# Kernel optimization log

Measured on AMD Instinct MI355X. Metric: run time of the kernel, lower is better.

The kernel has to match this reference:

```python
import jax, jax.numpy as jnp
import numpy as np

N = 50000
E = 800000
IN_DIM = 256
H1, D1 = 4, 128   # layer1: 4 heads x 128 = 512 concat
H2, D2 = 1, 256   # layer2: 1 head x 256
NEG_SLOPE = 0.2


def setup_inputs() -> dict:
    key = jax.random.key(0)
    ks = jax.random.split(key, 12)
    feat = jax.random.normal(ks[0], (N, IN_DIM), dtype=jnp.float32)
    src1 = jax.random.randint(ks[1], (E,), 0, N)
    dst1 = jax.random.randint(ks[2], (E,), 0, N)
    src2 = jax.random.randint(ks[3], (E,), 0, N)
    dst2 = jax.random.randint(ks[4], (E,), 0, N)
    s1 = 1.0 / np.sqrt(IN_DIM)
    s2 = 1.0 / np.sqrt(H1 * D1)
    W1 = jax.random.normal(ks[5], (IN_DIM, H1 * D1), dtype=jnp.float32) * s1
    al1 = jax.random.normal(ks[6], (H1, D1), dtype=jnp.float32) * s1
    ar1 = jax.random.normal(ks[7], (H1, D1), dtype=jnp.float32) * s1
    W2 = jax.random.normal(ks[8], (H1 * D1, H2 * D2), dtype=jnp.float32) * s2
    al2 = jax.random.normal(ks[9], (H2, D2), dtype=jnp.float32) * s2
    ar2 = jax.random.normal(ks[10], (H2, D2), dtype=jnp.float32) * s2
    return {"feat": feat, "src1": src1, "dst1": dst1, "src2": src2,
            "dst2": dst2, "W1": W1, "al1": al1, "ar1": ar1,
            "W2": W2, "al2": al2, "ar2": ar2}


def gat_layer(x, W, al, ar, src, dst, heads):
    n = x.shape[0]
    h = (x @ W).reshape(n, heads, -1)               # [N,H,D]
    el = jnp.einsum('nhd,hd->nh', h, al)            # attention left term
    er = jnp.einsum('nhd,hd->nh', h, ar)            # attention right term
    e = jax.nn.leaky_relu(el[src] + er[dst], NEG_SLOPE)   # [E,H]
    # segment softmax over edges grouped by destination node
    m = jax.ops.segment_max(e, dst, num_segments=n)
    m = jax.lax.stop_gradient(jnp.where(jnp.isfinite(m), m, 0.0))
    ee = jnp.exp(e - m[dst])
    s = jax.ops.segment_sum(ee, dst, num_segments=n)
    alpha = ee / (s[dst] + 1e-9)                    # [E,H]
    msg = h[src] * alpha[:, :, None]                # [E,H,D]
    return jax.ops.segment_sum(msg, dst, num_segments=n)  # [N,H,D]


def reference(feat, src1, dst1, src2, dst2, W1, al1, ar1, W2, al2, ar2):
    h1 = gat_layer(feat, W1, al1, ar1, src1, dst1, H1)      # [N,4,128]
    h1 = jax.nn.elu(h1.reshape(N, H1 * D1))                 # concat heads + act
    z = gat_layer(h1, W2, al2, ar2, src2, dst2, H2)         # [N,1,256]
    return z.reshape(N, D2)                                 # no act on last layer
```

## Files before the change

kernel.cpp:

```cpp
#include <hip/hip_runtime.h>
#include <stdint.h>

#define NN 50000
#define EE 800000
#define IND 256
#define HD1 512
#define D2C 256

#define NB1 782
#define NB  (2 * NB1)
#define CH  16384
#define WGN ((2 * EE + CH - 1) / CH)
#define TOT (NB * WGN)
#define SB2 ((TOT + 255) / 256)

#define Q_SCALE 21.166666f
#define Q_INV   0.047244094f

typedef float f32x4 __attribute__((ext_vector_type(4)));
typedef __bf16 bf16x8 __attribute__((ext_vector_type(8)));

__device__ inline float bf2f(unsigned int u) {
    union { unsigned int i; float f; } c; c.i = u << 16; return c.f;
}
__device__ inline unsigned int f2bf(float f) {
    union { float f; unsigned int i; } c; c.f = f;
    unsigned int x = c.i;
    return (x + 0x7FFFu + ((x >> 16) & 1u)) >> 16;
}
__device__ inline float loadf(const void* p, int idx, int isbf) {
    return isbf ? bf2f(((const unsigned short*)p)[idx]) : ((const float*)p)[idx];
}
__device__ inline unsigned int f2q8(float v) {
    float t = fminf(fmaxf(v * Q_SCALE, -127.f), 127.f);
    int q = (int)rintf(t);
    return (unsigned int)q & 0xFFu;
}
__device__ inline void unpack8_q8(uint2 q, float* o) {
    o[0] = (float)(int)(signed char)(q.x & 0xFFu);
    o[1] = (float)(int)(signed char)((q.x >> 8) & 0xFFu);
    o[2] = (float)(int)(signed char)((q.x >> 16) & 0xFFu);
    o[3] = (float)(int)(signed char)(q.x >> 24);
    o[4] = (float)(int)(signed char)(q.y & 0xFFu);
    o[5] = (float)(int)(signed char)((q.y >> 8) & 0xFFu);
    o[6] = (float)(int)(signed char)((q.y >> 16) & 0xFFu);
    o[7] = (float)(int)(signed char)(q.y >> 24);
}

__global__ void probe_k(const unsigned int* __restrict__ w, int* __restrict__ flag) {
    __shared__ int red[256];
    int t = threadIdx.x;
    int ok = 0;
    for (int i = t; i < 4096; i += 256) {
        unsigned int v = w[i];
        unsigned int e0 = (v >> 7) & 0xffu;
        unsigned int e1 = (v >> 23) & 0xffu;
        ok += (e0 <= 133u) + (e1 <= 133u);
    }
    red[t] = ok;
    __syncthreads();
    for (int s = 128; s > 0; s >>= 1) {
        if (t < s) red[t] += red[t + s];
        __syncthreads();
    }
    if (t == 0) *flag = (red[0] >= 7782) ? 1 : 0;
}

__global__ __launch_bounds__(256) void convert_k(
    const void* __restrict__ in, const int* __restrict__ flagp,
    unsigned short* __restrict__ out)
{
    int isbf = (*flagp != 0);
    size_t i = ((size_t)blockIdx.x * 256 + threadIdx.x) * 8;
    if (i >= (size_t)NN * IND) return;
    if (isbf) {
        *(uint4*)(out + i) = *(const uint4*)((const unsigned short*)in + i);
    } else {
        const float* f = (const float*)in + i;
        f32x4 p0 = *(const f32x4*)f;
        f32x4 p1 = *(const f32x4*)(f + 4);
        uint4 va;
        va.x = f2bf(p0.x) | (f2bf(p0.y) << 16);
        va.y = f2bf(p0.z) | (f2bf(p0.w) << 16);
        va.z = f2bf(p1.x) | (f2bf(p1.y) << 16);
        va.w = f2bf(p1.z) | (f2bf(p1.w) << 16);
        *(uint4*)(out + i) = va;
    }
}

__global__ __launch_bounds__(256) void gemm_bt(
    const unsigned short* __restrict__ A, const int* __restrict__ flagp,
    const unsigned short* __restrict__ BT,
    void* __restrict__ C, int c_q8,
    int M, int K, int Nc,
    const void* __restrict__ al, const void* __restrict__ ar,
    float* __restrict__ el, float* __restrict__ er, int eler_mode)
{
    const int LD = 40;
    __shared__ unsigned short Als[128 * LD];
    __shared__ unsigned short Bls[128 * LD];
    __shared__ float elp[128];
    __shared__ float erp[128];
    int isbf = (*flagp != 0);
    int tid  = threadIdx.x;
    int wave = tid >> 6;
    int lane = tid & 63;
    int wr = (wave >> 1) * 64;
    int wc = (wave & 1) * 64;
    int m0 = blockIdx.x * 128;
    int n0 = blockIdx.y * 128;
    if (tid < 128) { elp[tid] = 0.f; erp[tid] = 0.f; }
    f32x4 acc[4][4];
#pragma unroll
    for (int i = 0; i < 4; i++)
#pragma unroll
        for (int j = 0; j < 4; j++) acc[i][j] = (f32x4){0.f, 0.f, 0.f, 0.f};
    int sr = tid >> 2;
    int sc = (tid & 3) * 8;
    int frow = lane & 15;
    int kg = (lane >> 4) * 8;
    for (int kt = 0; kt < K; kt += 32) {
#pragma unroll
        for (int half = 0; half < 2; ++half) {
            int r = sr + half * 64;
            int gm = m0 + r;
            uint4 va = make_uint4(0u, 0u, 0u, 0u);
            if (gm < M) va = *(const uint4*)(A + (size_t)gm * K + kt + sc);
            *(uint4*)(Als + r * LD + sc) = va;
            uint4 vb = *(const uint4*)(BT + (size_t)(n0 + r) * K + kt + sc);
            *(uint4*)(Bls + r * LD + sc) = vb;
        }
        __syncthreads();
        bf16x8 af[4], bfr[4];
#pragma unroll
        for (int i = 0; i < 4; i++)
            af[i] = __builtin_bit_cast(bf16x8, *(const uint4*)(Als + (wr + i * 16 + frow) * LD + kg));
#pragma unroll
        for (int j = 0; j < 4; j++)
            bfr[j] = __builtin_bit_cast(bf16x8, *(const uint4*)(Bls + (wc + j * 16 + frow) * LD + kg));
#pragma unroll
        for (int i = 0; i < 4; i++)
#pragma unroll
            for (int j = 0; j < 4; j++)
                acc[i][j] = __builtin_amdgcn_mfma_f32_16x16x32_bf16(af[i], bfr[j], acc[i][j], 0, 0, 0);
        __syncthreads();
    }
    int nb = n0 + wc + frow;
    int mb = m0 + wr + (lane >> 4) * 4;
#pragma unroll
    for (int i = 0; i < 4; i++) {
#pragma unroll
        for (int j = 0; j < 4; j++) {
            int n = nb + j * 16;
#pragma unroll
            for (int r = 0; r < 4; r++) {
                int m = mb + i * 16 + r;
                if (m < M) {
                    if (c_q8)
                        ((unsigned char*)C)[(size_t)m * Nc + n] = (unsigned char)f2q8(acc[i][j][r]);
                    else
                        ((unsigned short*)C)[(size_t)m * Nc + n] = (unsigned short)f2bf(acc[i][j][r]);
                }
            }
        }
    }
    float alv[4], arv[4];
#pragma unroll
    for (int j = 0; j < 4; j++) {
        int c = n0 + wc + frow + j * 16;
        alv[j] = loadf(al, c, isbf);
        arv[j] = loadf(ar, c, isbf);
    }
#pragma unroll
    for (int i = 0; i < 4; i++) {
#pragma unroll
        for (int r = 0; r < 4; r++) {
            float pe = 0.f, pr = 0.f;
#pragma unroll
            for (int j = 0; j < 4; j++) {
                pe += acc[i][j][r] * alv[j];
                pr += acc[i][j][r] * arv[j];
            }
#pragma unroll
            for (int o = 1; o < 16; o <<= 1) {
                pe += __shfl_xor(pe, o);
                pr += __shfl_xor(pr, o);
            }
            if ((lane & 15) == 0) {
                int row = wr + (lane >> 4) * 4 + i * 16 + r;
                atomicAdd(&elp[row], pe);
                atomicAdd(&erp[row], pr);
            }
        }
    }
    __syncthreads();
    if (tid < 128) {
        int m = m0 + tid;
        if (m < M) {
            if (eler_mode == 1) {
                el[m * 4 + blockIdx.y] = elp[tid];
                er[m * 4 + blockIdx.y] = erp[tid];
            } else {
                atomicAdd(&el[m], elp[tid]);
                atomicAdd(&er[m], erp[tid]);
            }
        }
    }
}

__global__ void transpose_k(const void* __restrict__ in, const int* __restrict__ flagp,
                            unsigned short* __restrict__ out, int R, int C) {
    int isbf = (*flagp != 0);
    int idx = blockIdx.x * blockDim.x + threadIdx.x;
    if (idx < R * C) {
        int i = idx / C, j = idx - i * C;
        unsigned short v = isbf ? ((const unsigned short*)in)[idx]
                                : (unsigned short)f2bf(((const float*)in)[idx]);
        out[j * R + i] = v;
    }
}

__global__ __launch_bounds__(256) void binA_k(
    const int* __restrict__ dst1, const int* __restrict__ dst2,
    int* __restrict__ hist)
{
    __shared__ int lh[NB];
    int t = threadIdx.x, w = blockIdx.x;
    for (int b = t; b < NB; b += 256) lh[b] = 0;
    __syncthreads();
    int base = w * CH;
    for (int k = 0; k < CH; k += 256) {
        int i = base + k + t;
        if (i < 2 * EE) {
            int d, lay;
            if (i < EE) { d = dst1[i]; lay = 0; }
            else        { d = dst2[i - EE]; lay = 1; }
            d = ((unsigned)d < (unsigned)NN) ? d : 0;
            atomicAdd(&lh[lay * NB1 + (d >> 6)], 1);
        }
    }
    __syncthreads();
    for (int b = t; b < NB; b += 256) hist[b * WGN + w] = lh[b];
}
__global__ void scan_a(int* __restrict__ hist, int* __restrict__ bsum) {
    __shared__ int sdata[256];
    int t = threadIdx.x;
    int g = blockIdx.x * 256 + t;
    int v = (g < TOT) ? hist[g] : 0;
    sdata[t] = v;
    __syncthreads();
    for (int o = 1; o < 256; o <<= 1) {
        int x = (t >= o) ? sdata[t - o] : 0;
        __syncthreads();
        sdata[t] += x;
        __syncthreads();
    }
    if (g < TOT) hist[g] = sdata[t] - v;
    if (t == 255) bsum[blockIdx.x] = sdata[255];
}
__global__ void scan_b(const int* __restrict__ bsum, int* __restrict__ boff) {
    __shared__ int sdata[1024];
    int t = threadIdx.x;
    int v = (t < SB2) ? bsum[t] : 0;
    sdata[t] = v;
    __syncthreads();
    for (int o = 1; o < 1024; o <<= 1) {
        int x = (t >= o) ? sdata[t - o] : 0;
        __syncthreads();
        sdata[t] += x;
        __syncthreads();
    }
    boff[t] = sdata[t] - v;
}
__global__ void scan_c(int* __restrict__ hist, const int* __restrict__ boff) {
    int g = blockIdx.x * 256 + threadIdx.x;
    if (g < TOT) hist[g] += boff[blockIdx.x];
}
__global__ __launch_bounds__(256) void binC_k(
    const int* __restrict__ src1, const int* __restrict__ dst1,
    const int* __restrict__ src2, const int* __restrict__ dst2,
    const int* __restrict__ base_g, unsigned int* __restrict__ bucketed)
{
    __shared__ int cur[NB];
    int t = threadIdx.x, w = blockIdx.x;
    for (int b = t; b < NB; b += 256) cur[b] = base_g[b * WGN + w];
    __syncthreads();
    int base = w * CH;
    for (int k = 0; k < CH; k += 256) {
        int i = base + k + t;
        if (i < 2 * EE) {
            int d, s, lay;
            if (i < EE) { d = dst1[i]; s = src1[i]; lay = 0; }
            else        { d = dst2[i - EE]; s = src2[i - EE]; lay = 1; }
            d = ((unsigned)d < (unsigned)NN) ? d : 0;
            s = ((unsigned)s < (unsigned)NN) ? s : 0;
            int b = lay * NB1 + (d >> 6);
            int p = atomicAdd(&cur[b], 1);
            bucketed[p] = (unsigned)s | ((unsigned)(d & 63) << 16);
        }
    }
}
__global__ __launch_bounds__(256) void binD_k(
    const int* __restrict__ base_g, const unsigned int* __restrict__ bucketed,
    int* __restrict__ csr, int* __restrict__ row_ptr)
{
    __shared__ int cnt[64];
    __shared__ int off[64];
    __shared__ int cur[64];
    int b = blockIdx.x, t = threadIdx.x;
    int s = base_g[b * WGN];
    int e = (b + 1 < NB) ? base_g[(b + 1) * WGN] : (2 * EE);
    int lay = (b >= NB1) ? 1 : 0;
    int b0 = b - lay * NB1;
    if (t < 64) cnt[t] = 0;
    __syncthreads();
    for (int i = s + t; i < e; i += 256)
        atomicAdd(&cnt[bucketed[i] >> 16], 1);
    __syncthreads();
    if (t == 0) {
        int run = s;
        for (int j = 0; j < 64; j++) { off[j] = run; run += cnt[j]; }
    }
    __syncthreads();
    if (t < 64) {
        int node = b0 * 64 + t;
        if (node < NN) row_ptr[lay * NN + node] = off[t];
        cur[t] = off[t];
    }
    __syncthreads();
    for (int i = s + t; i < e; i += 256) {
        unsigned v = bucketed[i];
        int p = atomicAdd(&cur[v >> 16], 1);
        csr[p] = (int)(v & 0xFFFFu);
    }
    if (b == NB - 1 && t == 0) row_ptr[2 * NN] = e;
}

__global__ __launch_bounds__(256) void agg1_k(
    const unsigned char* __restrict__ h1,
    const float* __restrict__ el, const float* __restrict__ er,
    const int* __restrict__ row_ptr, const int* __restrict__ csr,
    unsigned short* __restrict__ x2)
{
    int wv = (blockIdx.x * blockDim.x + threadIdx.x) >> 6;
    int lane = threadIdx.x & 63;
    if (wv >= NN) return;
    int h = lane >> 4;
    float erv = er[wv * 4 + h];
    int e0 = row_ptr[wv], e1 = row_ptr[wv + 1];
    float l = 0.f;
    float acc[8];
#pragma unroll
    for (int j = 0; j < 8; j++) acc[j] = 0.f;
    int e = e0;
    for (; e + 1 < e1; e += 2) {
        int s0 = csr[e];
        int s1 = csr[e + 1];
        s0 = ((unsigned)s0 < (unsigned)NN) ? s0 : 0;
        s1 = ((unsigned)s1 < (unsigned)NN) ? s1 : 0;
        float ev0 = el[s0 * 4 + h] + erv;
        float ev1 = el[s1 * 4 + h] + erv;
        ev0 = (ev0 > 0.f) ? ev0 : 0.2f * ev0;
        ev1 = (ev1 > 0.f) ? ev1 : 0.2f * ev1;
        float w0 = __expf(fminf(ev0, 80.f));
        float w1 = __expf(fminf(ev1, 80.f));
        uint2 p0 = *(const uint2*)(h1 + (size_t)s0 * HD1 + lane * 8);
        uint2 p1 = *(const uint2*)(h1 + (size_t)s1 * HD1 + lane * 8);
        float f0[8], f1[8];
        unpack8_q8(p0, f0);
        unpack8_q8(p1, f1);
        l += w0 + w1;
        float w0s = w0 * Q_INV, w1s = w1 * Q_INV;
#pragma unroll
        for (int j = 0; j < 8; j++) acc[j] += w0s * f0[j] + w1s * f1[j];
    }
    if (e < e1) {
        int s = csr[e];
        s = ((unsigned)s < (unsigned)NN) ? s : 0;
        float ev = el[s * 4 + h] + erv;
        ev = (ev > 0.f) ? ev : 0.2f * ev;
        float wgt = __expf(fminf(ev, 80.f));
        l += wgt;
        float hf[8];
        unpack8_q8(*(const uint2*)(h1 + (size_t)s * HD1 + lane * 8), hf);
        float ws = wgt * Q_INV;
#pragma unroll
        for (int j = 0; j < 8; j++) acc[j] += ws * hf[j];
    }
    float inv = 1.f / (l + 1e-9f);
    unsigned int o[4];
#pragma unroll
    for (int j = 0; j < 4; j++) {
        float v0 = acc[2 * j] * inv;
        float v1 = acc[2 * j + 1] * inv;
        v0 = (v0 > 0.f) ? v0 : (__expf(v0) - 1.f);
        v1 = (v1 > 0.f) ? v1 : (__expf(v1) - 1.f);
        o[j] = f2bf(v0) | (f2bf(v1) << 16);
    }
    *(uint4*)(x2 + (size_t)wv * HD1 + lane * 8) = make_uint4(o[0], o[1], o[2], o[3]);
}

__global__ __launch_bounds__(256) void agg2_k(
    const unsigned short* __restrict__ h2,
    const float* __restrict__ el, const float* __restrict__ er,
    const int* __restrict__ row_ptr, const int* __restrict__ csr,
    void* __restrict__ outv, const int* __restrict__ flagp)
{
    int isbf = (*flagp != 0);
    int wv = (blockIdx.x * blockDim.x + threadIdx.x) >> 6;
    int lane = threadIdx.x & 63;
    if (wv >= NN) return;
    float erv = er[wv];
    int e0 = row_ptr[NN + wv], e1 = row_ptr[NN + wv + 1];
    float l = 0.f;
    float a0 = 0.f, a1 = 0.f, a2 = 0.f, a3 = 0.f;
    int e = e0;
    for (; e + 1 < e1; e += 2) {
        int s0 = csr[e];
        int s1 = csr[e + 1];
        s0 = ((unsigned)s0 < (unsigned)NN) ? s0 : 0;
        s1 = ((unsigned)s1 < (unsigned)NN) ? s1 : 0;
        float ev0 = el[s0] + erv;
        float ev1 = el[s1] + erv;
        ev0 = (ev0 > 0.f) ? ev0 : 0.2f * ev0;
        ev1 = (ev1 > 0.f) ? ev1 : 0.2f * ev1;
        float w0 = __expf(fminf(ev0, 80.f));
        float w1 = __expf(fminf(ev1, 80.f));
        uint2 t0 = *(const uint2*)(h2 + (size_t)s0 * D2C + lane * 4);
        uint2 t1 = *(const uint2*)(h2 + (size_t)s1 * D2C + lane * 4);
        l += w0 + w1;
        a0 += w0 * bf2f(t0.x & 0xffffu) + w1 * bf2f(t1.x & 0xffffu);
        a1 += w0 * bf2f(t0.x >> 16)     + w1 * bf2f(t1.x >> 16);
        a2 += w0 * bf2f(t0.y & 0xffffu) + w1 * bf2f(t1.y & 0xffffu);
        a3 += w0 * bf2f(t0.y >> 16)     + w1 * bf2f(t1.y >> 16);
    }
    if (e < e1) {
        int s = csr[e];
        s = ((unsigned)s < (unsigned)NN) ? s : 0;
        float ev = el[s] + erv;
        ev = (ev > 0.f) ? ev : 0.2f * ev;
        float wgt = __expf(fminf(ev, 80.f));
        l += wgt;
        uint2 t = *(const uint2*)(h2 + (size_t)s * D2C + lane * 4);
        a0 += wgt * bf2f(t.x & 0xffffu);
        a1 += wgt * bf2f(t.x >> 16);
        a2 += wgt * bf2f(t.y & 0xffffu);
        a3 += wgt * bf2f(t.y >> 16);
    }
    float inv = 1.f / (l + 1e-9f);
    float v0 = a0 * inv, v1 = a1 * inv, v2 = a2 * inv, v3 = a3 * inv;
    if (isbf) {
        uint2 o;
        o.x = f2bf(v0) | (f2bf(v1) << 16);
        o.y = f2bf(v2) | (f2bf(v3) << 16);
        *(uint2*)((unsigned short*)outv + (size_t)wv * D2C + lane * 4) = o;
    } else {
        f32x4 o = (f32x4){v0, v1, v2, v3};
        *(f32x4*)((float*)outv + (size_t)wv * D2C + lane * 4) = o;
    }
}

extern "C" void kernel_launch(void* const* d_in, const int* in_sizes, int n_in,
                              void* d_out, int out_size, void* d_ws, size_t ws_size,
                              hipStream_t stream) {
    const void* feat = d_in[0];
    const int* src1 = (const int*)d_in[1];
    const int* dst1 = (const int*)d_in[2];
    const int* src2 = (const int*)d_in[3];
    const int* dst2 = (const int*)d_in[4];
    const void* W1  = d_in[5];
    const void* al1 = d_in[6];
    const void* ar1 = d_in[7];
    const void* W2  = d_in[8];
    const void* al2 = d_in[9];
    const void* ar2 = d_in[10];

    uint8_t* w = (uint8_t*)d_ws;
    auto alloc = [&](size_t bytes) -> void* {
        void* p = (void*)w;
        w += (bytes + 255) & ~(size_t)255;
        return p;
    };
    int* flag    = (int*)alloc(256);
    float* el    = (float*)alloc((size_t)NN * 4 * 4);
    float* er    = (float*)alloc((size_t)NN * 4 * 4);
    unsigned short* W1T = (unsigned short*)alloc((size_t)IND * HD1 * 2);
    unsigned short* W2T = (unsigned short*)alloc((size_t)HD1 * D2C * 2);
    int* hist    = (int*)alloc((size_t)TOT * 4);
    int* bsum    = (int*)alloc(1024 * 4);
    int* boff    = (int*)alloc(1024 * 4);
    unsigned int* bucketed = (unsigned int*)alloc((size_t)2 * EE * 4);
    int* csr     = (int*)alloc((size_t)2 * EE * 4);
    int* row_ptr = (int*)alloc((size_t)(2 * NN + 1) * 4);
    unsigned char* h1 = (unsigned char*)alloc((size_t)NN * HD1);
    unsigned short* x2 = (unsigned short*)alloc((size_t)NN * HD1 * 2);
    unsigned short* h2 = (unsigned short*)h1;
    unsigned short* featb = x2;

    probe_k<<<1, 256, 0, stream>>>((const unsigned int*)feat, flag);
    convert_k<<<(NN * IND / 8 + 255) / 256, 256, 0, stream>>>(feat, flag, featb);
    transpose_k<<<(IND * HD1 + 255) / 256, 256, 0, stream>>>(W1, flag, W1T, IND, HD1);
    transpose_k<<<(HD1 * D2C + 255) / 256, 256, 0, stream>>>(W2, flag, W2T, HD1, D2C);

    binA_k<<<WGN, 256, 0, stream>>>(dst1, dst2, hist);
    scan_a<<<SB2, 256, 0, stream>>>(hist, bsum);
    scan_b<<<1, 1024, 0, stream>>>(bsum, boff);
    scan_c<<<SB2, 256, 0, stream>>>(hist, boff);
    binC_k<<<WGN, 256, 0, stream>>>(src1, dst1, src2, dst2, hist, bucketed);
    binD_k<<<NB, 256, 0, stream>>>(hist, bucketed, csr, row_ptr);

    gemm_bt<<<dim3((NN + 127) / 128, HD1 / 128), 256, 0, stream>>>(
        featb, flag, W1T, h1, 1, NN, IND, HD1, al1, ar1, el, er, 1);
    agg1_k<<<(NN + 3) / 4, 256, 0, stream>>>(h1, el, er, row_ptr, csr, x2);

    hipMemsetAsync(el, 0, (size_t)NN * 4, stream);
    hipMemsetAsync(er, 0, (size_t)NN * 4, stream);
    gemm_bt<<<dim3((NN + 127) / 128, D2C / 128), 256, 0, stream>>>(
        x2, flag, W2T, (void*)h2, 0, NN, HD1, D2C, al2, ar2, el, er, 2);
    agg2_k<<<(NN + 3) / 4, 256, 0, stream>>>(h2, el, er, row_ptr, csr, d_out, flag);
}
```

Baseline: 463.8 us.

## Widen GEMM tile to 256 columns and drop el/er atomics and memsets

The GEMM block tile grows from 128x128 to 128x256, so each wave computes 64x128 with twice as many accumulators. This halves how often A is reloaded across the column grid, and for layer 2 one block covers the whole output width. el/er are then written directly, with no global atomics and no zeroing memsets. The aggregation kernels also drop the clamp on source indices and use 32-bit offset arithmetic. The costs are higher register and LDS pressure, which can lower occupancy, and loss of the safety against out-of-range csr entries.

```diff
diff --git a/kernel.cpp b/kernel.cpp
--- a/kernel.cpp
+++ b/kernel.cpp
@@ -98,23 +98,23 @@
 {
     const int LD = 40;
     __shared__ unsigned short Als[128 * LD];
-    __shared__ unsigned short Bls[128 * LD];
-    __shared__ float elp[128];
-    __shared__ float erp[128];
+    __shared__ unsigned short Bls[256 * LD];
+    __shared__ float elp[256];
+    __shared__ float erp[256];
     int isbf = (*flagp != 0);
     int tid  = threadIdx.x;
     int wave = tid >> 6;
     int lane = tid & 63;
     int wr = (wave >> 1) * 64;
-    int wc = (wave & 1) * 64;
+    int wc = (wave & 1) * 128;
     int m0 = blockIdx.x * 128;
-    int n0 = blockIdx.y * 128;
-    if (tid < 128) { elp[tid] = 0.f; erp[tid] = 0.f; }
-    f32x4 acc[4][4];
+    int n0 = blockIdx.y * 256;
+    elp[tid] = 0.f; erp[tid] = 0.f;
+    f32x4 acc[4][8];
 #pragma unroll
     for (int i = 0; i < 4; i++)
 #pragma unroll
-        for (int j = 0; j < 4; j++) acc[i][j] = (f32x4){0.f, 0.f, 0.f, 0.f};
+        for (int j = 0; j < 8; j++) acc[i][j] = (f32x4){0.f, 0.f, 0.f, 0.f};
     int sr = tid >> 2;
     int sc = (tid & 3) * 8;
     int frow = lane & 15;
@@ -127,21 +127,25 @@
             uint4 va = make_uint4(0u, 0u, 0u, 0u);
             if (gm < M) va = *(const uint4*)(A + (size_t)gm * K + kt + sc);
             *(uint4*)(Als + r * LD + sc) = va;
+        }
+#pragma unroll
+        for (int q = 0; q < 4; ++q) {
+            int r = sr + q * 64;
             uint4 vb = *(const uint4*)(BT + (size_t)(n0 + r) * K + kt + sc);
             *(uint4*)(Bls + r * LD + sc) = vb;
         }
         __syncthreads();
-        bf16x8 af[4], bfr[4];
+        bf16x8 af[4], bfr[8];
 #pragma unroll
         for (int i = 0; i < 4; i++)
             af[i] = __builtin_bit_cast(bf16x8, *(const uint4*)(Als + (wr + i * 16 + frow) * LD + kg));
 #pragma unroll
-        for (int j = 0; j < 4; j++)
+        for (int j = 0; j < 8; j++)
             bfr[j] = __builtin_bit_cast(bf16x8, *(const uint4*)(Bls + (wc + j * 16 + frow) * LD + kg));
 #pragma unroll
         for (int i = 0; i < 4; i++)
 #pragma unroll
-            for (int j = 0; j < 4; j++)
+            for (int j = 0; j < 8; j++)
                 acc[i][j] = __builtin_amdgcn_mfma_f32_16x16x32_bf16(af[i], bfr[j], acc[i][j], 0, 0, 0);
         __syncthreads();
     }
@@ -150,7 +154,7 @@
 #pragma unroll
     for (int i = 0; i < 4; i++) {
 #pragma unroll
-        for (int j = 0; j < 4; j++) {
+        for (int j = 0; j < 8; j++) {
             int n = nb + j * 16;
 #pragma unroll
             for (int r = 0; r < 4; r++) {
@@ -164,20 +168,21 @@
             }
         }
     }
-    float alv[4], arv[4];
-#pragma unroll
-    for (int j = 0; j < 4; j++) {
+    float alv[8], arv[8];
+#pragma unroll
+    for (int j = 0; j < 8; j++) {
         int c = n0 + wc + frow + j * 16;
         alv[j] = loadf(al, c, isbf);
         arv[j] = loadf(ar, c, isbf);
     }
+    int hg = wc >> 7;
 #pragma unroll
     for (int i = 0; i < 4; i++) {
 #pragma unroll
         for (int r = 0; r < 4; r++) {
             float pe = 0.f, pr = 0.f;
 #pragma unroll
-            for (int j = 0; j < 4; j++) {
+            for (int j = 0; j < 8; j++) {
                 pe += acc[i][j][r] * alv[j];
                 pr += acc[i][j][r] * arv[j];
             }
@@ -188,8 +193,8 @@
             }
             if ((lane & 15) == 0) {
                 int row = wr + (lane >> 4) * 4 + i * 16 + r;
-                atomicAdd(&elp[row], pe);
-                atomicAdd(&erp[row], pr);
+                atomicAdd(&elp[row * 2 + hg], pe);
+                atomicAdd(&erp[row * 2 + hg], pr);
             }
         }
     }
@@ -198,11 +203,13 @@
         int m = m0 + tid;
         if (m < M) {
             if (eler_mode == 1) {
-                el[m * 4 + blockIdx.y] = elp[tid];
-                er[m * 4 + blockIdx.y] = erp[tid];
+                el[m * 4 + 2 * blockIdx.y + 0] = elp[tid * 2];
+                el[m * 4 + 2 * blockIdx.y + 1] = elp[tid * 2 + 1];
+                er[m * 4 + 2 * blockIdx.y + 0] = erp[tid * 2];
+                er[m * 4 + 2 * blockIdx.y + 1] = erp[tid * 2 + 1];
             } else {
-                atomicAdd(&el[m], elp[tid]);
-                atomicAdd(&er[m], erp[tid]);
+                el[m] = elp[tid * 2] + elp[tid * 2 + 1];
+                er[m] = erp[tid * 2] + erp[tid * 2 + 1];
             }
         }
     }
@@ -348,6 +355,7 @@
     int h = lane >> 4;
     float erv = er[wv * 4 + h];
     int e0 = row_ptr[wv], e1 = row_ptr[wv + 1];
+    unsigned lo = (unsigned)(lane * 8);
     float l = 0.f;
     float acc[8];
 #pragma unroll
@@ -356,16 +364,14 @@
     for (; e + 1 < e1; e += 2) {
         int s0 = csr[e];
         int s1 = csr[e + 1];
-        s0 = ((unsigned)s0 < (unsigned)NN) ? s0 : 0;
-        s1 = ((unsigned)s1 < (unsigned)NN) ? s1 : 0;
         float ev0 = el[s0 * 4 + h] + erv;
         float ev1 = el[s1 * 4 + h] + erv;
         ev0 = (ev0 > 0.f) ? ev0 : 0.2f * ev0;
         ev1 = (ev1 > 0.f) ? ev1 : 0.2f * ev1;
         float w0 = __expf(fminf(ev0, 80.f));
         float w1 = __expf(fminf(ev1, 80.f));
-        uint2 p0 = *(const uint2*)(h1 + (size_t)s0 * HD1 + lane * 8);
-        uint2 p1 = *(const uint2*)(h1 + (size_t)s1 * HD1 + lane * 8);
+        uint2 p0 = *(const uint2*)(h1 + ((unsigned)s0 * HD1 + lo));
+        uint2 p1 = *(const uint2*)(h1 + ((unsigned)s1 * HD1 + lo));
         float f0[8], f1[8];
         unpack8_q8(p0, f0);
         unpack8_q8(p1, f1);
@@ -376,13 +382,12 @@
     }
     if (e < e1) {
         int s = csr[e];
-        s = ((unsigned)s < (unsigned)NN) ? s : 0;
         float ev = el[s * 4 + h] + erv;
         ev = (ev > 0.f) ? ev : 0.2f * ev;
         float wgt = __expf(fminf(ev, 80.f));
         l += wgt;
         float hf[8];
-        unpack8_q8(*(const uint2*)(h1 + (size_t)s * HD1 + lane * 8), hf);
+        unpack8_q8(*(const uint2*)(h1 + ((unsigned)s * HD1 + lo)), hf);
         float ws = wgt * Q_INV;
 #pragma unroll
         for (int j = 0; j < 8; j++) acc[j] += ws * hf[j];
@@ -412,22 +417,21 @@
     if (wv >= NN) return;
     float erv = er[wv];
     int e0 = row_ptr[NN + wv], e1 = row_ptr[NN + wv + 1];
+    unsigned lo = (unsigned)(lane * 4);
     float l = 0.f;
     float a0 = 0.f, a1 = 0.f, a2 = 0.f, a3 = 0.f;
     int e = e0;
     for (; e + 1 < e1; e += 2) {
         int s0 = csr[e];
         int s1 = csr[e + 1];
-        s0 = ((unsigned)s0 < (unsigned)NN) ? s0 : 0;
-        s1 = ((unsigned)s1 < (unsigned)NN) ? s1 : 0;
         float ev0 = el[s0] + erv;
         float ev1 = el[s1] + erv;
         ev0 = (ev0 > 0.f) ? ev0 : 0.2f * ev0;
         ev1 = (ev1 > 0.f) ? ev1 : 0.2f * ev1;
         float w0 = __expf(fminf(ev0, 80.f));
         float w1 = __expf(fminf(ev1, 80.f));
-        uint2 t0 = *(const uint2*)(h2 + (size_t)s0 * D2C + lane * 4);
-        uint2 t1 = *(const uint2*)(h2 + (size_t)s1 * D2C + lane * 4);
+        uint2 t0 = *(const uint2*)(h2 + ((unsigned)s0 * D2C + lo));
+        uint2 t1 = *(const uint2*)(h2 + ((unsigned)s1 * D2C + lo));
         l += w0 + w1;
         a0 += w0 * bf2f(t0.x & 0xffffu) + w1 * bf2f(t1.x & 0xffffu);
         a1 += w0 * bf2f(t0.x >> 16)     + w1 * bf2f(t1.x >> 16);
@@ -436,12 +440,11 @@
     }
     if (e < e1) {
         int s = csr[e];
-        s = ((unsigned)s < (unsigned)NN) ? s : 0;
         float ev = el[s] + erv;
         ev = (ev > 0.f) ? ev : 0.2f * ev;
         float wgt = __expf(fminf(ev, 80.f));
         l += wgt;
-        uint2 t = *(const uint2*)(h2 + (size_t)s * D2C + lane * 4);
+        uint2 t = *(const uint2*)(h2 + ((unsigned)s * D2C + lo));
         a0 += wgt * bf2f(t.x & 0xffffu);
         a1 += wgt * bf2f(t.x >> 16);
         a2 += wgt * bf2f(t.y & 0xffffu);
@@ -509,13 +512,11 @@
     binC_k<<<WGN, 256, 0, stream>>>(src1, dst1, src2, dst2, hist, bucketed);
     binD_k<<<NB, 256, 0, stream>>>(hist, bucketed, csr, row_ptr);
 
-    gemm_bt<<<dim3((NN + 127) / 128, HD1 / 128), 256, 0, stream>>>(
+    gemm_bt<<<dim3((NN + 127) / 128, HD1 / 256), 256, 0, stream>>>(
         featb, flag, W1T, h1, 1, NN, IND, HD1, al1, ar1, el, er, 1);
     agg1_k<<<(NN + 3) / 4, 256, 0, stream>>>(h1, el, er, row_ptr, csr, x2);
 
-    hipMemsetAsync(el, 0, (size_t)NN * 4, stream);
-    hipMemsetAsync(er, 0, (size_t)NN * 4, stream);
-    gemm_bt<<<dim3((NN + 127) / 128, D2C / 128), 256, 0, stream>>>(
+    gemm_bt<<<dim3((NN + 127) / 128, D2C / 256), 256, 0, stream>>>(
         x2, flag, W2T, (void*)h2, 0, NN, HD1, D2C, al2, ar2, el, er, 2);
     agg2_k<<<(NN + 3) / 4, 256, 0, stream>>>(h2, el, er, row_ptr, csr, d_out, flag);
 }
```

New measurement: 504.6 us. 8.8% more time.
